# Kernel tuning notes

Measured on AMD Instinct MI355X. Metric: run time of the kernel, lower is better.

## Reference

```python
import jax, jax.numpy as jnp
import numpy as np

N_HEADS = 16
HEAD_DIM = 64
EMB = 1024
B, S = 2, 2048


def setup_inputs() -> dict:
    key = jax.random.key(0)
    ks = jax.random.split(key, 8)
    inner = N_HEADS * HEAD_DIM
    return {
        "query": jax.random.normal(ks[0], (B, S, EMB), dtype=jnp.float32),
        "key": jax.random.normal(ks[1], (B, S, EMB), dtype=jnp.float32),
        "value": jax.random.normal(ks[2], (B, S, EMB), dtype=jnp.float32),
        "positional_mask": jnp.ones((B, S), dtype=bool),
        "future_mask": 1,
        # torch nn.Linear weight layout: (out_features, in_features)
        "Wq": jax.random.normal(ks[3], (inner, EMB), dtype=jnp.float32) * 0.02,
        "Wk": jax.random.normal(ks[4], (inner, EMB), dtype=jnp.float32) * 0.02,
        "Wv": jax.random.normal(ks[5], (inner, EMB), dtype=jnp.float32) * 0.02,
        "Wo": jax.random.normal(ks[6], (EMB, inner), dtype=jnp.float32) * 0.02,
        "bo": jax.random.normal(ks[7], (EMB,), dtype=jnp.float32) * 0.02,
    }


def reference(query, key, value, positional_mask, future_mask, Wq, Wk, Wv, Wo, bo):
    batch, seq = query.shape[:2]
    # project and split heads: (B, S, H, D)
    q = (query @ Wq.T).reshape(batch, seq, N_HEADS, HEAD_DIM)
    k = (key @ Wk.T).reshape(batch, seq, N_HEADS, HEAD_DIM)
    v = (value @ Wv.T).reshape(batch, seq, N_HEADS, HEAD_DIM)
    scale = 1.0 / np.sqrt(HEAD_DIM).astype(np.float32)
    # (B, H, Sq, Sk)
    weights = jnp.einsum("bqhd,bkhd->bhqk", q, k) * scale
    neg_inf = jnp.float32(-jnp.inf)
    # additive key-position mask
    reweight = jnp.where(positional_mask, jnp.float32(0.0), neg_inf)  # (B, S)
    weights = weights + reweight[:, None, None, :]
    if future_mask:
        causal = jnp.triu(jnp.full((seq, seq), neg_inf, dtype=weights.dtype), k=1)
        weights = weights + causal
    weights = jax.nn.softmax(weights, axis=-1)
    out = jnp.einsum("bhqk,bkhd->bqhd", weights, v).reshape(batch, seq, -1)
    return out @ Wo.T + bo
```

## Files before the change

### kernel.cpp

```cpp
#include <hip/hip_runtime.h>
#include <hip/hip_bf16.h>
#include <math.h>

#define EMB    1024
#define NH     16
#define HD     64
#define BATCH  2
#define SEQ    2048
#define MTOK   (BATCH * SEQ)

typedef __bf16 bf16_t;
typedef __bf16 bf16x8 __attribute__((ext_vector_type(8)));
typedef __bf16 bf16x4 __attribute__((ext_vector_type(4)));
typedef float  f32x4  __attribute__((ext_vector_type(4)));

#define NEG_BIG (-1.0e30f)

#define GLD16(g, l) __builtin_amdgcn_global_load_lds(                     \
    (const __attribute__((address_space(1))) void*)(g),                   \
    (__attribute__((address_space(3))) void*)(l), 16, 0, 0)

__device__ inline bf16x8 ld_frag64(const bf16_t* __restrict__ p) {
    const bf16x4 lo = *(const bf16x4*)p;
    const bf16x4 hi = *(const bf16x4*)(p + 4);
    bf16x8 r;
#pragma unroll
    for (int j = 0; j < 4; ++j) { r[j] = lo[j]; r[j + 4] = hi[j]; }
    return r;
}

__global__ __launch_bounds__(256) void cast_bf16(
    const float* __restrict__ q, const float* __restrict__ k,
    const float* __restrict__ v, const float* __restrict__ wq,
    const float* __restrict__ wk, const float* __restrict__ wv,
    const float* __restrict__ wo, bf16_t* __restrict__ ws)
{
    const size_t g = ((size_t)blockIdx.x * 256 + threadIdx.x) * 8;
    const size_t BIG = (size_t)1 << 22;
    const size_t SML = (size_t)1 << 20;
    const float* src;
    bf16_t* dst;
    size_t off;
    if (g < 3 * BIG) {
        const int s = (int)(g >> 22);
        src = s == 0 ? q : (s == 1 ? k : v);
        dst = ws + (size_t)s * BIG;
        off = g & (BIG - 1);
    } else {
        const size_t h = g - 3 * BIG;
        const int s = (int)(h >> 20);
        src = s == 0 ? wq : (s == 1 ? wk : (s == 2 ? wv : wo));
        dst = ws + 3 * BIG + (size_t)s * SML;
        off = h & (SML - 1);
    }
    const f32x4 f0 = *(const f32x4*)(src + off);
    const f32x4 f1 = *(const f32x4*)(src + off + 4);
    bf16x8 r;
#pragma unroll
    for (int j = 0; j < 4; ++j) { r[j] = (bf16_t)f0[j]; r[j + 4] = (bf16_t)f1[j]; }
    *(bf16x8*)(dst + off) = r;
}

template<int BM, int BN, bool OUTF32>
__global__ __launch_bounds__(256) void gemm_dma(
    const bf16_t* __restrict__ A, const bf16_t* __restrict__ Wb,
    const float* __restrict__ bias, void* __restrict__ Cp,
    size_t sA, size_t sW, size_t sC, float ascale)
{
    constexpr int K = EMB, N = EMB;
    constexpr int MT = BM / 32, NT = BN / 32;
    constexpr int IA = BM / 64, IB = BN / 64;
    constexpr int nT = K / 32;
    __shared__ __align__(16) bf16_t As[3][BM * 32];
    __shared__ __align__(16) bf16_t Bs[3][BN * 32];

    const int tid  = threadIdx.x;
    const int wave = tid >> 6;
    const int lane = tid & 63;
    const int l15  = lane & 15;
    const int quad = lane >> 4;
    const int z    = blockIdx.z;
    A  += (size_t)z * sA;
    Wb += (size_t)z * sW;

    const int m0 = blockIdx.y * BM;
    const int n0 = blockIdx.x * BN;
    const int wm = (wave >> 1) * (BM / 2);
    const int wn = (wave & 1) * (BN / 2);

    const int lrow = lane >> 2;
    const int scol = ((lane & 3) ^ (lrow & 3)) * 8;
    const bf16_t* gA = A  + (size_t)(m0 + wave * (BM / 4) + lrow) * K + scol;
    const bf16_t* gB = Wb + (size_t)(n0 + wave * (BN / 4) + lrow) * K + scol;
    const int loffA = wave * (BM / 4) * 32;
    const int loffB = wave * (BN / 4) * 32;

    f32x4 acc[MT][NT] = {};
    const int xq = (quad ^ (l15 & 3)) * 8;

    auto stage = [&](int t, int b3) {
        const size_t ko = (size_t)t * 32;
#pragma unroll
        for (int i = 0; i < IA; ++i)
            GLD16(gA + ko + (size_t)i * 16 * K, &As[b3][loffA + i * 512]);
#pragma unroll
        for (int i = 0; i < IB; ++i)
            GLD16(gB + ko + (size_t)i * 16 * K, &Bs[b3][loffB + i * 512]);
    };

    stage(0, 0);
    stage(1, 1);

    int cur = 0;
    for (int t = 0; t < nT; ++t) {
        if (t == nT - 1) {
            asm volatile("s_waitcnt vmcnt(0)" ::: "memory");
        } else {
            asm volatile("s_waitcnt vmcnt(%0)" :: "n"(IA + IB) : "memory");
        }
        __builtin_amdgcn_s_barrier();

        bf16x8 af[MT], bfr[NT];
#pragma unroll
        for (int mt = 0; mt < MT; ++mt)
            af[mt] = *(const bf16x8*)&As[cur][(wm + mt * 16 + l15) * 32 + xq];
#pragma unroll
        for (int nt = 0; nt < NT; ++nt)
            bfr[nt] = *(const bf16x8*)&Bs[cur][(wn + nt * 16 + l15) * 32 + xq];
        __builtin_amdgcn_s_setprio(1);
#pragma unroll
        for (int mt = 0; mt < MT; ++mt)
#pragma unroll
            for (int nt = 0; nt < NT; ++nt)
                acc[mt][nt] = __builtin_amdgcn_mfma_f32_16x16x32_bf16(
                    af[mt], bfr[nt], acc[mt][nt], 0, 0, 0);
        __builtin_amdgcn_s_setprio(0);

        if (t + 2 < nT) {
            int b3 = cur + 2; if (b3 >= 3) b3 -= 3;
            stage(t + 2, b3);
        }
        if (++cur == 3) cur = 0;
    }

    const size_t cb = (size_t)z * sC;
    const float sc = (z == 0) ? ascale : 1.0f;
#pragma unroll
    for (int nt = 0; nt < NT; ++nt) {
        const int col = n0 + wn + nt * 16 + l15;
        const float bv = bias ? bias[col] : 0.0f;
#pragma unroll
        for (int mt = 0; mt < MT; ++mt) {
#pragma unroll
            for (int r = 0; r < 4; ++r) {
                const int row = m0 + wm + mt * 16 + quad * 4 + r;
                const float v = acc[mt][nt][r] * sc + bv;
                if constexpr (OUTF32) ((float*) Cp)[cb + (size_t)row * N + col] = v;
                else                  ((bf16_t*)Cp)[cb + (size_t)row * N + col] = (bf16_t)v;
            }
        }
    }
}

__global__ __launch_bounds__(256) void attn_flash(
    const bf16_t* __restrict__ Q, const bf16_t* __restrict__ Km,
    const bf16_t* __restrict__ V, bf16_t* __restrict__ O)
{
    __shared__ __align__(16) bf16_t Ks[2][64 * 64];
    __shared__ __align__(16) bf16_t Vs[2][64][76];
    __shared__ bf16_t Pb[4][16 * 68];
    __shared__ bf16_t Ob[4][16 * 72];

    const int tid  = threadIdx.x;
    const int wave = tid >> 6;
    const int lane = tid & 63;
    const int l15  = lane & 15;
    const int quad = lane >> 4;
    const int b = blockIdx.z, h = blockIdx.y;

    const bf16_t* Qb = Q  + ((size_t)b * SEQ) * EMB + h * HD;
    const bf16_t* Kb = Km + ((size_t)b * SEQ) * EMB + h * HD;
    const bf16_t* Vb = V  + ((size_t)b * SEQ) * EMB + h * HD;

    const int krow = lane >> 3;
    const int kcol = ((lane & 7) ^ krow) * 8;
    const int vk   = wave * 16;
    bf16_t* P = Pb[wave];
    const int sw = l15 & 7;

    for (int ph = 0; ph < 2; ++ph) {
        const int qi = (ph == 0) ? (int)blockIdx.x : 31 - (int)blockIdx.x;
        const int qbase = qi * 64 + wave * 16;
        const int qg = qbase + l15;
        const int nkt = qi + 1;

        const bf16x8 qlo = *(const bf16x8*)(Qb + (size_t)(qbase + l15) * EMB + quad * 8);
        const bf16x8 qhi = *(const bf16x8*)(Qb + (size_t)(qbase + l15) * EMB + 32 + quad * 8);

        float m_s = NEG_BIG, l_s = 0.0f;
        f32x4 o[4] = {};

        __syncthreads();
#pragma unroll
        for (int i = 0; i < 2; ++i) {
            const int r0 = wave * 16 + i * 8;
            GLD16(Kb + (size_t)(r0 + krow) * EMB + kcol, &Ks[0][r0 * 64]);
        }
        {
            bf16x4 vr[4];
#pragma unroll
            for (int t = 0; t < 4; ++t)
#pragma unroll
                for (int j = 0; j < 4; ++j)
                    vr[t][j] = Vb[(size_t)(vk + t * 4 + j) * EMB + lane];
#pragma unroll
            for (int t = 0; t < 4; ++t)
                *(bf16x4*)&Vs[0][lane][vk + t * 4] = vr[t];
        }

        for (int kt = 0; kt < nkt; ++kt) {
            const int cur = kt & 1, nb = cur ^ 1;
            const int kb = kt * 64;
            __syncthreads();

            bf16x4 vr[4];
            const bool more = (kt + 1) < nkt;
            if (more) {
                const int kb1 = kb + 64;
#pragma unroll
                for (int i = 0; i < 2; ++i) {
                    const int r0 = wave * 16 + i * 8;
                    GLD16(Kb + (size_t)(kb1 + r0 + krow) * EMB + kcol, &Ks[nb][r0 * 64]);
                }
#pragma unroll
                for (int t = 0; t < 4; ++t)
#pragma unroll
                    for (int j = 0; j < 4; ++j)
                        vr[t][j] = Vb[(size_t)(kb1 + vk + t * 4 + j) * EMB + lane];
            }

            f32x4 s[4];
            __builtin_amdgcn_s_setprio(1);
#pragma unroll
            for (int t2 = 0; t2 < 4; ++t2) {
                const int row = t2 * 16 + l15;
                const bf16x8 klo = *(const bf16x8*)&Ks[cur][row * 64 + ((quad ^ sw) * 8)];
                const bf16x8 khi = *(const bf16x8*)&Ks[cur][row * 64 + (((4 + quad) ^ sw) * 8)];
                f32x4 a = {};
                a = __builtin_amdgcn_mfma_f32_16x16x32_bf16(klo, qlo, a, 0, 0, 0);
                a = __builtin_amdgcn_mfma_f32_16x16x32_bf16(khi, qhi, a, 0, 0, 0);
                s[t2] = a;
            }
            __builtin_amdgcn_s_setprio(0);

            if (more) {
#pragma unroll
                for (int t = 0; t < 4; ++t)
                    *(bf16x4*)&Vs[nb][lane][vk + t * 4] = vr[t];
            }

            float sc[16];
#pragma unroll
            for (int t2 = 0; t2 < 4; ++t2)
#pragma unroll
                for (int r = 0; r < 4; ++r)
                    sc[t2 * 4 + r] = s[t2][r];
            if (kt == nkt - 1) {
#pragma unroll
                for (int t2 = 0; t2 < 4; ++t2)
#pragma unroll
                    for (int r = 0; r < 4; ++r)
                        if (kb + t2 * 16 + quad * 4 + r > qg)
                            sc[t2 * 4 + r] = NEG_BIG;
            }
            const float a0 = fmaxf(fmaxf(sc[0],  sc[1]),  sc[2]);
            const float a1 = fmaxf(fmaxf(sc[3],  sc[4]),  sc[5]);
            const float a2 = fmaxf(fmaxf(sc[6],  sc[7]),  sc[8]);
            const float a3 = fmaxf(fmaxf(sc[9],  sc[10]), sc[11]);
            const float a4 = fmaxf(fmaxf(sc[12], sc[13]), sc[14]);
            float mx = fmaxf(fmaxf(fmaxf(fmaxf(a0, a1), a2), fmaxf(a3, a4)), sc[15]);
            mx = fmaxf(mx, __shfl_xor(mx, 16, 64));
            mx = fmaxf(mx, __shfl_xor(mx, 32, 64));
            if (!__all(mx - m_s <= 11.5f)) {
                const float mnew  = fmaxf(m_s, mx);
                const float alpha = __builtin_amdgcn_exp2f(m_s - mnew);
                l_s *= alpha;
#pragma unroll
                for (int dt = 0; dt < 4; ++dt)
#pragma unroll
                    for (int r = 0; r < 4; ++r) o[dt][r] *= alpha;
                m_s = mnew;
            }
            float e[16], rs = 0.0f;
#pragma unroll
            for (int j = 0; j < 16; ++j) {
                e[j] = __builtin_amdgcn_exp2f(sc[j] - m_s);
                rs += e[j];
            }
            rs += __shfl_xor(rs, 16, 64);
            rs += __shfl_xor(rs, 32, 64);
            l_s += rs;

#pragma unroll
            for (int t2 = 0; t2 < 4; ++t2) {
                bf16x4 p4;
#pragma unroll
                for (int r = 0; r < 4; ++r) p4[r] = (bf16_t)e[t2 * 4 + r];
                *(bf16x4*)&P[l15 * 68 + t2 * 16 + quad * 4] = p4;
            }
            __asm__ volatile("s_waitcnt lgkmcnt(0)" ::: "memory");
            const bf16x8 pb0 = ld_frag64(&P[l15 * 68 + quad * 8]);
            const bf16x8 pb1 = ld_frag64(&P[l15 * 68 + 32 + quad * 8]);

            __builtin_amdgcn_s_setprio(1);
#pragma unroll
            for (int dt = 0; dt < 4; ++dt) {
                const bf16x8 va0 = ld_frag64(&Vs[cur][dt * 16 + l15][quad * 8]);
                const bf16x8 va1 = ld_frag64(&Vs[cur][dt * 16 + l15][32 + quad * 8]);
                o[dt] = __builtin_amdgcn_mfma_f32_16x16x32_bf16(va0, pb0, o[dt], 0, 0, 0);
                o[dt] = __builtin_amdgcn_mfma_f32_16x16x32_bf16(va1, pb1, o[dt], 0, 0, 0);
            }
            __builtin_amdgcn_s_setprio(0);
        }

        const float inv = 1.0f / l_s;
        bf16_t* OT = Ob[wave];
#pragma unroll
        for (int dt = 0; dt < 4; ++dt) {
            bf16x4 pk;
#pragma unroll
            for (int r = 0; r < 4; ++r) pk[r] = (bf16_t)(o[dt][r] * inv);
            *(bf16x4*)&OT[l15 * 72 + dt * 16 + quad * 4] = pk;
        }
        __asm__ volatile("s_waitcnt lgkmcnt(0)" ::: "memory");
        const bf16x8 r0 = *(const bf16x8*)&OT[l15 * 72 + quad * 16];
        const bf16x8 r1 = *(const bf16x8*)&OT[l15 * 72 + quad * 16 + 8];
        bf16_t* dst = O + ((size_t)b * SEQ + qbase + l15) * EMB + h * HD + quad * 16;
        *(bf16x8*)dst       = r0;
        *(bf16x8*)(dst + 8) = r1;
    }
}

extern "C" void kernel_launch(void* const* d_in, const int* in_sizes, int n_in,
                              void* d_out, int out_size, void* d_ws, size_t ws_size,
                              hipStream_t stream)
{
    const float* query = (const float*)d_in[0];
    const float* key   = (const float*)d_in[1];
    const float* value = (const float*)d_in[2];
    const float* Wq = (const float*)d_in[5];
    const float* Wk = (const float*)d_in[6];
    const float* Wv = (const float*)d_in[7];
    const float* Wo = (const float*)d_in[8];
    const float* bo = (const float*)d_in[9];

    const size_t BIG = (size_t)1 << 22, SML = (size_t)1 << 20;
    bf16_t* ws  = (bf16_t*)d_ws;
    bf16_t* qc  = ws;
    bf16_t* kc  = qc + BIG;
    bf16_t* vc  = kc + BIG;
    bf16_t* wqc = vc + BIG;
    bf16_t* wkc = wqc + SML;
    bf16_t* wvc = wkc + SML;
    bf16_t* woc = wvc + SML;
    bf16_t* Qp  = woc + SML;
    bf16_t* Kp  = Qp + BIG;
    bf16_t* Vp  = Kp + BIG;
    bf16_t* Ab  = Vp + BIG;

    const dim3 blk(256);
    const float QSCALE = 0.18033688011112042f;

    cast_bf16<<<dim3(8192), blk, 0, stream>>>(query, key, value, Wq, Wk, Wv, Wo, ws);

    gemm_dma<128, 128, false><<<dim3(EMB / 128, MTOK / 128, 3), blk, 0, stream>>>(
        qc, wqc, nullptr, Qp, BIG, SML, BIG, QSCALE);

    attn_flash<<<dim3(SEQ / 128, NH, BATCH), blk, 0, stream>>>(Qp, Kp, Vp, Ab);

    gemm_dma<64, 64, true><<<dim3(EMB / 64, MTOK / 64, 1), blk, 0, stream>>>(
        Ab, woc, bo, (float*)d_out, 0, 0, 0, 1.0f);
}
```

Before: 232.9 us.

## Retile QKV GEMM to 256x256 tiles and split-K the output projection

The QKV projection moves to a specialized kernel with 512 threads, 256x256 tiles, BK=64 double buffering and a remapped block order grouped for L2 reuse. The output projection now uses 128x128 tiles with split-K of two halves that write fp32 partials into reused workspace, followed by a separate kernel that sums the partials and adds the bias. The intent is higher MFMA utilization and better wave fill on the machine, at the cost of an extra kernel launch and extra fp32 partial traffic.

```diff
diff --git a/kernel.cpp b/kernel.cpp
--- a/kernel.cpp
+++ b/kernel.cpp
@@ -61,51 +61,147 @@
     *(bf16x8*)(dst + off) = r;
 }
 
-template<int BM, int BN, bool OUTF32>
-__global__ __launch_bounds__(256) void gemm_dma(
-    const bf16_t* __restrict__ A, const bf16_t* __restrict__ Wb,
-    const float* __restrict__ bias, void* __restrict__ Cp,
-    size_t sA, size_t sW, size_t sC, float ascale)
+__global__ __launch_bounds__(512) void gemm_qkv(
+    const bf16_t* __restrict__ A0, const bf16_t* __restrict__ W0,
+    bf16_t* __restrict__ Cp, size_t sA, size_t sW, size_t sC, float ascale)
 {
     constexpr int K = EMB, N = EMB;
-    constexpr int MT = BM / 32, NT = BN / 32;
-    constexpr int IA = BM / 64, IB = BN / 64;
-    constexpr int nT = K / 32;
-    __shared__ __align__(16) bf16_t As[3][BM * 32];
-    __shared__ __align__(16) bf16_t Bs[3][BN * 32];
+    __shared__ __align__(16) bf16_t As[2][256 * 64];
+    __shared__ __align__(16) bf16_t Bs[2][256 * 64];
 
     const int tid  = threadIdx.x;
     const int wave = tid >> 6;
     const int lane = tid & 63;
     const int l15  = lane & 15;
     const int quad = lane >> 4;
-    const int z    = blockIdx.z;
-    A  += (size_t)z * sA;
-    Wb += (size_t)z * sW;
-
-    const int m0 = blockIdx.y * BM;
-    const int n0 = blockIdx.x * BN;
-    const int wm = (wave >> 1) * (BM / 2);
-    const int wn = (wave & 1) * (BN / 2);
+
+    const int bid = blockIdx.x;
+    const int wg  = (bid & 7) * 24 + (bid >> 3);
+    const int y   = wg & 15;
+    const int pan = wg >> 4;
+    const int x   = pan & 3;
+    const int z   = pan >> 2;
+
+    const bf16_t* A  = A0 + (size_t)z * sA;
+    const bf16_t* Wb = W0 + (size_t)z * sW;
+    const int m0 = y * 256, n0 = x * 256;
+    const int wm = (wave >> 2) * 128;
+    const int wn = (wave & 3) * 64;
+
+    const int srow = lane >> 3;
+    const int scol = ((lane & 7) ^ srow) * 8;
+    const bf16_t* gA = A  + (size_t)(m0 + wave * 32 + srow) * K + scol;
+    const bf16_t* gB = Wb + (size_t)(n0 + wave * 32 + srow) * K + scol;
+    const int loff = wave * 32 * 64;
+
+    f32x4 acc[8][4] = {};
+
+    auto stage = [&](int t, int b) {
+        const size_t ko = (size_t)t * 64;
+#pragma unroll
+        for (int i = 0; i < 4; ++i) {
+            GLD16(gA + ko + (size_t)i * 8 * K, &As[b][loff + i * 512]);
+            GLD16(gB + ko + (size_t)i * 8 * K, &Bs[b][loff + i * 512]);
+        }
+    };
+
+    stage(0, 0);
+
+    for (int t = 0; t < 16; ++t) {
+        const int cur = t & 1;
+        __builtin_amdgcn_s_barrier();
+        if (t + 1 < 16) {
+            stage(t + 1, cur ^ 1);
+            asm volatile("s_waitcnt vmcnt(8)" ::: "memory");
+        } else {
+            asm volatile("s_waitcnt vmcnt(0)" ::: "memory");
+        }
+        __builtin_amdgcn_s_barrier();
+
+#pragma unroll
+        for (int h = 0; h < 2; ++h) {
+            bf16x8 af[8], bfr[4];
+#pragma unroll
+            for (int mt = 0; mt < 8; ++mt) {
+                const int r = wm + mt * 16 + l15;
+                const int c8 = (quad + h * 4) ^ (l15 & 7);
+                af[mt] = *(const bf16x8*)&As[cur][r * 64 + c8 * 8];
+            }
+#pragma unroll
+            for (int nt = 0; nt < 4; ++nt) {
+                const int r = wn + nt * 16 + l15;
+                const int c8 = (quad + h * 4) ^ (l15 & 7);
+                bfr[nt] = *(const bf16x8*)&Bs[cur][r * 64 + c8 * 8];
+            }
+            __builtin_amdgcn_s_setprio(1);
+#pragma unroll
+            for (int mt = 0; mt < 8; ++mt)
+#pragma unroll
+                for (int nt = 0; nt < 4; ++nt)
+                    acc[mt][nt] = __builtin_amdgcn_mfma_f32_16x16x32_bf16(
+                        af[mt], bfr[nt], acc[mt][nt], 0, 0, 0);
+            __builtin_amdgcn_s_setprio(0);
+        }
+    }
+
+    bf16_t* C = Cp + (size_t)z * sC;
+    const float sc = (z == 0) ? ascale : 1.0f;
+#pragma unroll
+    for (int nt = 0; nt < 4; ++nt) {
+        const int col = n0 + wn + nt * 16 + l15;
+#pragma unroll
+        for (int mt = 0; mt < 8; ++mt) {
+#pragma unroll
+            for (int r = 0; r < 4; ++r) {
+                const int row = m0 + wm + mt * 16 + quad * 4 + r;
+                C[(size_t)row * N + col] = (bf16_t)(acc[mt][nt][r] * sc);
+            }
+        }
+    }
+}
+
+__global__ __launch_bounds__(256) void gemm_wo(
+    const bf16_t* __restrict__ A, const bf16_t* __restrict__ Wb,
+    float* __restrict__ P0, float* __restrict__ P1)
+{
+    constexpr int K = EMB, N = EMB;
+    constexpr int nT = 16;
+    __shared__ __align__(16) bf16_t As[3][128 * 32];
+    __shared__ __align__(16) bf16_t Bs[3][128 * 32];
+
+    const int tid  = threadIdx.x;
+    const int wave = tid >> 6;
+    const int lane = tid & 63;
+    const int l15  = lane & 15;
+    const int quad = lane >> 4;
+
+    const int bid = blockIdx.x;
+    const int wg  = (bid & 7) * 64 + (bid >> 3);
+    const int y   = wg & 31;
+    const int pan = wg >> 5;
+    const int x   = pan & 7;
+    const int z   = pan >> 3;
+
+    const int m0 = y * 128, n0 = x * 128;
+    const int kb = z * 512;
+    const int wm = (wave >> 1) * 64;
+    const int wn = (wave & 1) * 64;
 
     const int lrow = lane >> 2;
     const int scol = ((lane & 3) ^ (lrow & 3)) * 8;
-    const bf16_t* gA = A  + (size_t)(m0 + wave * (BM / 4) + lrow) * K + scol;
-    const bf16_t* gB = Wb + (size_t)(n0 + wave * (BN / 4) + lrow) * K + scol;
-    const int loffA = wave * (BM / 4) * 32;
-    const int loffB = wave * (BN / 4) * 32;
-
-    f32x4 acc[MT][NT] = {};
+    const bf16_t* gA = A  + (size_t)(m0 + wave * 32 + lrow) * K + kb + scol;
+    const bf16_t* gB = Wb + (size_t)(n0 + wave * 32 + lrow) * K + kb + scol;
+    const int loff = wave * 1024;
+
+    f32x4 acc[4][4] = {};
     const int xq = (quad ^ (l15 & 3)) * 8;
 
     auto stage = [&](int t, int b3) {
         const size_t ko = (size_t)t * 32;
-#pragma unroll
-        for (int i = 0; i < IA; ++i)
-            GLD16(gA + ko + (size_t)i * 16 * K, &As[b3][loffA + i * 512]);
-#pragma unroll
-        for (int i = 0; i < IB; ++i)
-            GLD16(gB + ko + (size_t)i * 16 * K, &Bs[b3][loffB + i * 512]);
+        GLD16(gA + ko, &As[b3][loff]);
+        GLD16(gA + ko + (size_t)16 * K, &As[b3][loff + 512]);
+        GLD16(gB + ko, &Bs[b3][loff]);
+        GLD16(gB + ko + (size_t)16 * K, &Bs[b3][loff + 512]);
     };
 
     stage(0, 0);
@@ -113,25 +209,22 @@
 
     int cur = 0;
     for (int t = 0; t < nT; ++t) {
-        if (t == nT - 1) {
-            asm volatile("s_waitcnt vmcnt(0)" ::: "memory");
-        } else {
-            asm volatile("s_waitcnt vmcnt(%0)" :: "n"(IA + IB) : "memory");
-        }
+        if (t == nT - 1) asm volatile("s_waitcnt vmcnt(0)" ::: "memory");
+        else             asm volatile("s_waitcnt vmcnt(4)" ::: "memory");
         __builtin_amdgcn_s_barrier();
 
-        bf16x8 af[MT], bfr[NT];
-#pragma unroll
-        for (int mt = 0; mt < MT; ++mt)
+        bf16x8 af[4], bfr[4];
+#pragma unroll
+        for (int mt = 0; mt < 4; ++mt)
             af[mt] = *(const bf16x8*)&As[cur][(wm + mt * 16 + l15) * 32 + xq];
 #pragma unroll
-        for (int nt = 0; nt < NT; ++nt)
+        for (int nt = 0; nt < 4; ++nt)
             bfr[nt] = *(const bf16x8*)&Bs[cur][(wn + nt * 16 + l15) * 32 + xq];
         __builtin_amdgcn_s_setprio(1);
 #pragma unroll
-        for (int mt = 0; mt < MT; ++mt)
-#pragma unroll
-            for (int nt = 0; nt < NT; ++nt)
+        for (int mt = 0; mt < 4; ++mt)
+#pragma unroll
+            for (int nt = 0; nt < 4; ++nt)
                 acc[mt][nt] = __builtin_amdgcn_mfma_f32_16x16x32_bf16(
                     af[mt], bfr[nt], acc[mt][nt], 0, 0, 0);
         __builtin_amdgcn_s_setprio(0);
@@ -143,23 +236,37 @@
         if (++cur == 3) cur = 0;
     }
 
-    const size_t cb = (size_t)z * sC;
-    const float sc = (z == 0) ? ascale : 1.0f;
-#pragma unroll
-    for (int nt = 0; nt < NT; ++nt) {
+    float* C = z ? P1 : P0;
+#pragma unroll
+    for (int nt = 0; nt < 4; ++nt) {
         const int col = n0 + wn + nt * 16 + l15;
-        const float bv = bias ? bias[col] : 0.0f;
-#pragma unroll
-        for (int mt = 0; mt < MT; ++mt) {
+#pragma unroll
+        for (int mt = 0; mt < 4; ++mt)
 #pragma unroll
             for (int r = 0; r < 4; ++r) {
                 const int row = m0 + wm + mt * 16 + quad * 4 + r;
-                const float v = acc[mt][nt][r] * sc + bv;
-                if constexpr (OUTF32) ((float*) Cp)[cb + (size_t)row * N + col] = v;
-                else                  ((bf16_t*)Cp)[cb + (size_t)row * N + col] = (bf16_t)v;
-            }
-        }
-    }
+                C[(size_t)row * N + col] = acc[mt][nt][r];
+            }
+    }
+}
+
+__global__ __launch_bounds__(256) void combine_bias(
+    const float* __restrict__ p0, const float* __restrict__ p1,
+    const float* __restrict__ bias, float* __restrict__ out)
+{
+    const size_t g = ((size_t)blockIdx.x * 256 + threadIdx.x) * 8;
+    const int col = (int)(g & (EMB - 1));
+    const f32x4 a0 = *(const f32x4*)(p0 + g);
+    const f32x4 a1 = *(const f32x4*)(p0 + g + 4);
+    const f32x4 b0 = *(const f32x4*)(p1 + g);
+    const f32x4 b1 = *(const f32x4*)(p1 + g + 4);
+    const f32x4 c0 = *(const f32x4*)(bias + col);
+    const f32x4 c1 = *(const f32x4*)(bias + col + 4);
+    f32x4 r0, r1;
+#pragma unroll
+    for (int j = 0; j < 4; ++j) { r0[j] = a0[j] + b0[j] + c0[j]; r1[j] = a1[j] + b1[j] + c1[j]; }
+    *(f32x4*)(out + g)     = r0;
+    *(f32x4*)(out + g + 4) = r1;
 }
 
 __global__ __launch_bounds__(256) void attn_flash(
@@ -367,17 +474,21 @@
     bf16_t* Kp  = Qp + BIG;
     bf16_t* Vp  = Kp + BIG;
     bf16_t* Ab  = Vp + BIG;
+    float*  P0  = (float*)qc;
+    float*  P1  = (float*)Qp;
 
     const dim3 blk(256);
     const float QSCALE = 0.18033688011112042f;
 
     cast_bf16<<<dim3(8192), blk, 0, stream>>>(query, key, value, Wq, Wk, Wv, Wo, ws);
 
-    gemm_dma<128, 128, false><<<dim3(EMB / 128, MTOK / 128, 3), blk, 0, stream>>>(
-        qc, wqc, nullptr, Qp, BIG, SML, BIG, QSCALE);
+    gemm_qkv<<<dim3(192), dim3(512), 0, stream>>>(
+        qc, wqc, Qp, BIG, SML, BIG, QSCALE);
 
     attn_flash<<<dim3(SEQ / 128, NH, BATCH), blk, 0, stream>>>(Qp, Kp, Vp, Ab);
 
-    gemm_dma<64, 64, true><<<dim3(EMB / 64, MTOK / 64, 1), blk, 0, stream>>>(
-        Ab, woc, bo, (float*)d_out, 0, 0, 0, 1.0f);
-}
+    gemm_wo<<<dim3(512), blk, 0, stream>>>(Ab, woc, P0, P1);
+
+    combine_bias<<<dim3(2048), blk, 0, stream>>>(P0, P1, bo, (float*)d_out);
+    (void)vc;
+}
```

After: 239.3 us. 1.03x slower.
